# Performance work log

Hardware: AMD Instinct MI355X
Metric: run time of the kernel (lower is better)

Reference implementation:

```python
import jax, jax.numpy as jnp
import numpy as np
import math


def setup_inputs() -> dict:
    key = jax.random.key(0)
    k1, k2, k3, k4 = jax.random.split(key, 4)
    B, L, H, D = 2, 4096, 8, 64
    factor = 5
    U = factor * int(np.ceil(np.log(L)))  # 45 = sample_k = n_top
    return {
        "queries": jax.random.normal(k1, (B, L, H, D), dtype=jnp.float32),
        "keys": jax.random.normal(k2, (B, L, H, D), dtype=jnp.float32),
        "values": jax.random.normal(k3, (B, L, H, D), dtype=jnp.float32),
        "index_sample": jax.random.randint(k4, (L, U), 0, L),  # sampled key ids per query
    }


def reference(queries, keys, values, index_sample):
    # ProbAttention forward, mask_flag=False (non-causal ProbSparse attention).
    B, L_Q, H, D = queries.shape
    L_K = keys.shape[1]
    Q = jnp.transpose(queries, (0, 2, 1, 3))  # (B,H,L_Q,D)
    K = jnp.transpose(keys, (0, 2, 1, 3))     # (B,H,L_K,D)
    V = jnp.transpose(values, (0, 2, 1, 3))   # (B,H,L_K,D)
    n_top = index_sample.shape[1]             # U = factor*ceil(ln(L_K)) = sample_k = n_top

    # --- _prob_QK: score each query against a random subset of keys ---
    K_sample = K[:, :, index_sample, :]                     # (B,H,L_Q,sample_k,D)
    Q_K_sample = jnp.einsum('bhqd,bhqsd->bhqs', Q, K_sample)
    # sparsity measure M = max - mean (sum divided by full L_K, as in source)
    M = Q_K_sample.max(-1) - Q_K_sample.sum(-1) / L_K       # (B,H,L_Q)
    _, M_top = jax.lax.top_k(M, n_top)                      # (B,H,n_top)

    # full attention scores only for the selected top queries
    Q_reduce = jnp.take_along_axis(Q, M_top[..., None], axis=2)  # (B,H,n_top,D)
    scale = 1.0 / math.sqrt(D)
    scores = jnp.einsum('bhud,bhkd->bhuk', Q_reduce, K) * scale  # (B,H,n_top,L_K)
    attn = jax.nn.softmax(scores, axis=-1)

    # --- initial context (mask_flag=False): cumulative sum of V ---
    context = jnp.cumsum(V, axis=2)                         # (B,H,L_Q,D)

    # --- scatter attention outputs into the top-query rows ---
    update = jnp.einsum('bhuk,bhkd->bhud', attn, V)         # (B,H,n_top,D)
    bi = jnp.arange(B)[:, None, None]
    hi = jnp.arange(H)[None, :, None]
    context = context.at[bi, hi, M_top].set(update)

    return jnp.transpose(context, (0, 2, 1, 3))             # (B,L_Q,H,D)
```

## Files before the change

### kernel.cpp

```cpp
#include <hip/hip_runtime.h>
#include <math.h>

#define BB 2
#define LL 4096
#define HH 8
#define DD 64
#define UU 45
#define TILE 128
#define NTILES (LL / TILE)

#define NC 64
#define CK (LL / NC)
#define KSTR 68
#define SSTR 68

__device__ __forceinline__ int qkv_idx(int b, int l, int h, int d) {
    return ((b * LL + l) * HH + h) * DD + d;
}

__global__ __launch_bounds__(256) void k_computeM(
        const float* __restrict__ Q, const float* __restrict__ K,
        const int* __restrict__ idx, float* __restrict__ M) {
    int w = (blockIdx.x * blockDim.x + threadIdx.x) >> 6;
    int lane = threadIdx.x & 63;
    int q = w % LL;
    int bh = w / LL;
    int h = bh % HH, b = bh / HH;

    const float* Kbh = K + (size_t)(b * LL * HH + h) * DD;
    const size_t rowStride = (size_t)HH * DD;

    float qv = Q[qkv_idx(b, q, h, lane)];
    int myks = idx[q * UU + (lane < UU ? lane : 0)];

    int r = lane >> 4;
    int c16 = lane & 15;

    float q0 = __shfl(qv, c16 * 4 + 0, 64);
    float q1 = __shfl(qv, c16 * 4 + 1, 64);
    float q2 = __shfl(qv, c16 * 4 + 2, 64);
    float q3 = __shfl(qv, c16 * 4 + 3, 64);

    float mval = -INFINITY, sval = 0.f;
#pragma unroll
    for (int g = 0; g < 12; ++g) {
        int s = g * 4 + r;
        int ks = __shfl(myks, s, 64);
        const float4* kp = (const float4*)(Kbh + (size_t)ks * rowStride);
        float4 kk = kp[c16];
        float part = fmaf(kk.x, q0, fmaf(kk.y, q1, fmaf(kk.z, q2, kk.w * q3)));
        part += __shfl_xor(part, 8, 64);
        part += __shfl_xor(part, 4, 64);
        part += __shfl_xor(part, 2, 64);
        part += __shfl_xor(part, 1, 64);
        if (s < UU) { mval = fmaxf(mval, part); sval += part; }
    }
    mval = fmaxf(mval, __shfl_xor(mval, 16, 64));
    sval += __shfl_xor(sval, 16, 64);
    mval = fmaxf(mval, __shfl_xor(mval, 32, 64));
    sval += __shfl_xor(sval, 32, 64);
    if (lane == 0) M[bh * LL + q] = mval - sval * (1.0f / LL);
}

__global__ __launch_bounds__(1024) void k_topk(
        const float* __restrict__ M, int* __restrict__ Mtop) {
    int bh = blockIdx.x;
    int t = threadIdx.x;
    __shared__ unsigned keys[LL];
    __shared__ unsigned hist[256];
    __shared__ unsigned scanbuf[256];
    __shared__ unsigned sPrefix, sMask, sK, sBin;
    __shared__ int outCount, eqCount;
    __shared__ int eqIdx[64];

    for (int i = t; i < LL; i += 1024) {
        unsigned u = __float_as_uint(M[bh * LL + i]);
        keys[i] = (u & 0x80000000u) ? ~u : (u | 0x80000000u);
    }
    if (t == 0) { sPrefix = 0u; sMask = 0u; sK = UU; outCount = 0; eqCount = 0; }
    __syncthreads();

    for (int pass = 0; pass < 4; ++pass) {
        int shift = 24 - pass * 8;
        if (t < 256) hist[t] = 0u;
        __syncthreads();
        unsigned prefix = sPrefix, mask = sMask;
        for (int i = t; i < LL; i += 1024) {
            unsigned k = keys[i];
            if ((k & mask) == prefix)
                atomicAdd(&hist[(k >> shift) & 0xFFu], 1u);
        }
        __syncthreads();
        if (t < 256) scanbuf[t] = hist[t];
        __syncthreads();
        for (int off = 1; off < 256; off <<= 1) {
            unsigned v = 0u;
            if (t < 256 && t + off < 256) v = scanbuf[t + off];
            __syncthreads();
            if (t < 256) scanbuf[t] += v;
            __syncthreads();
        }
        if (t < 256) {
            unsigned k = sK;
            unsigned geq = scanbuf[t];
            unsigned gt = (t < 255) ? scanbuf[t + 1] : 0u;
            if (gt < k && geq >= k) sBin = (unsigned)t;
        }
        __syncthreads();
        if (t == 0) {
            unsigned b = sBin;
            unsigned gt = (b < 255u) ? scanbuf[b + 1] : 0u;
            sK -= gt;
            sPrefix |= (b << shift);
            sMask |= (0xFFu << shift);
        }
        __syncthreads();
    }
    unsigned T = sPrefix;
    int kEq = (int)sK;

    for (int i = t; i < LL; i += 1024) {
        unsigned k = keys[i];
        if (k > T) {
            int slot = atomicAdd(&outCount, 1);
            Mtop[bh * UU + slot] = i;
        } else if (k == T) {
            int e = atomicAdd(&eqCount, 1);
            if (e < 64) eqIdx[e] = i;
        }
    }
    __syncthreads();

    if (t == 0) {
        int base = outCount;
        int ec = eqCount;
        if (ec <= 64) {
            for (int s = 0; s < UU; ++s) {
                if (s >= kEq) break;
                int bi = -1, bv = LL + 2;
                for (int j = 0; j < ec; ++j) {
                    int v = eqIdx[j];
                    if (v < bv) { bv = v; bi = j; }
                }
                Mtop[bh * UU + base + s] = bv;
                eqIdx[bi] = LL + 2;
            }
        } else {
            int got = 0;
            for (int i = 0; i < LL && got < kEq; ++i)
                if (keys[i] == T) { Mtop[bh * UU + base + got] = i; ++got; }
        }
    }
}

__global__ __launch_bounds__(256) void k_tilesum(
        const float* __restrict__ V, float* __restrict__ tsum) {
    int blk = blockIdx.x;
    int tile = blk % NTILES;
    int bh = blk / NTILES;
    int h = bh % HH, b = bh / HH;
    int d = threadIdx.x & 63, g = threadIdx.x >> 6;
    const int CH = TILE / 4;
    int l0 = tile * TILE + g * CH;
    float acc = 0.f;
    for (int i = 0; i < CH; ++i) acc += V[qkv_idx(b, l0 + i, h, d)];
    __shared__ float red[4][DD];
    red[g][d] = acc;
    __syncthreads();
    if (g == 0) tsum[blk * DD + d] = red[0][d] + red[1][d] + red[2][d] + red[3][d];
}

__global__ void k_scantiles(float* __restrict__ tsum) {
    int bh = blockIdx.x;
    int d = threadIdx.x;
    float off = 0.f;
    for (int t = 0; t < NTILES; ++t) {
        int i = (bh * NTILES + t) * DD + d;
        float v = tsum[i];
        tsum[i] = off;
        off += v;
    }
}

__global__ __launch_bounds__(256) void k_cumsum(
        const float* __restrict__ V, const float* __restrict__ tsum,
        float* __restrict__ out) {
    int blk = blockIdx.x;
    int tile = blk % NTILES;
    int bh = blk / NTILES;
    int h = bh % HH, b = bh / HH;
    int d = threadIdx.x & 63, g = threadIdx.x >> 6;
    const int CH = TILE / 4;
    int l0 = tile * TILE + g * CH;

    __shared__ float red[4][DD];
    float acc = 0.f;
    for (int i = 0; i < CH; ++i) acc += V[qkv_idx(b, l0 + i, h, d)];
    red[g][d] = acc;
    __syncthreads();

    float off = tsum[blk * DD + d];
    for (int gg = 0; gg < g; ++gg) off += red[gg][d];

    float run = off;
    for (int i = 0; i < CH; ++i) {
        run += V[qkv_idx(b, l0 + i, h, d)];
        out[qkv_idx(b, l0 + i, h, d)] = run;
    }
}

__global__ __launch_bounds__(256) void k_attn_partial(
        const float* __restrict__ Q, const float* __restrict__ K,
        const float* __restrict__ V, const int* __restrict__ Mtop,
        float* __restrict__ mPart, float* __restrict__ lPart,
        float* __restrict__ Op) {
    int blk = blockIdx.x;
    int c = blk % NC;
    int bh = blk / NC;
    int h = bh % HH, b = bh / HH;
    int k0 = c * CK;
    int t = threadIdx.x;

    __shared__ float Qs[48 * KSTR];
    __shared__ float Ks[CK * KSTR];
    __shared__ float Ss[UU * SSTR];

    const size_t rowStride = (size_t)HH * DD;
    const float* Qbh = Q + (size_t)(b * LL * HH + h) * DD;
    const float* Kbh = K + (size_t)(b * LL * HH + h) * DD;
    const float* Vbh = V + (size_t)(b * LL * HH + h) * DD;

    for (int p = t; p < 48 * DD; p += 256) {
        int u = p >> 6, d = p & 63;
        float v = 0.f;
        if (u < UU) {
            int qi = Mtop[bh * UU + u];
            v = Qbh[(size_t)qi * rowStride + d] * 0.125f;
        }
        Qs[u * KSTR + d] = v;
    }
    for (int p = t; p < CK * 16; p += 256) {
        int row = p >> 4, i = p & 15;
        *(float4*)&Ks[row * KSTR + i * 4] =
            *(const float4*)&Kbh[(size_t)(k0 + row) * rowStride + i * 4];
    }
    __syncthreads();

    int kq = t & 15, uq = t >> 4;
    int u0 = uq * 3;
    float acc[3][4];
#pragma unroll
    for (int i = 0; i < 3; ++i)
#pragma unroll
        for (int j = 0; j < 4; ++j) acc[i][j] = 0.f;

#pragma unroll 4
    for (int dd = 0; dd < 16; ++dd) {
        float4 qf[3];
#pragma unroll
        for (int i = 0; i < 3; ++i)
            qf[i] = *(const float4*)&Qs[(u0 + i) * KSTR + dd * 4];
        float4 kf[4];
#pragma unroll
        for (int j = 0; j < 4; ++j)
            kf[j] = *(const float4*)&Ks[(kq + 16 * j) * KSTR + dd * 4];
#pragma unroll
        for (int i = 0; i < 3; ++i)
#pragma unroll
            for (int j = 0; j < 4; ++j) {
                acc[i][j] = fmaf(qf[i].x, kf[j].x, acc[i][j]);
                acc[i][j] = fmaf(qf[i].y, kf[j].y, acc[i][j]);
                acc[i][j] = fmaf(qf[i].z, kf[j].z, acc[i][j]);
                acc[i][j] = fmaf(qf[i].w, kf[j].w, acc[i][j]);
            }
    }
#pragma unroll
    for (int i = 0; i < 3; ++i) {
        int u = u0 + i;
        if (u < UU)
#pragma unroll
            for (int j = 0; j < 4; ++j) Ss[u * SSTR + kq + 16 * j] = acc[i][j];
    }
    __syncthreads();

    for (int p = t; p < CK * 16; p += 256) {
        int row = p >> 4, i = p & 15;
        *(float4*)&Ks[row * KSTR + i * 4] =
            *(const float4*)&Vbh[(size_t)(k0 + row) * rowStride + i * 4];
    }

    if (t < UU * 4) {
        int u = t >> 2, qq = t & 3;
        float mloc = -INFINITY;
        for (int j = 0; j < CK / 4; ++j)
            mloc = fmaxf(mloc, Ss[u * SSTR + qq + 4 * j]);
        mloc = fmaxf(mloc, __shfl_xor(mloc, 1, 64));
        mloc = fmaxf(mloc, __shfl_xor(mloc, 2, 64));
        float lloc = 0.f;
        for (int j = 0; j < CK / 4; ++j) {
            int kk = qq + 4 * j;
            float e = __expf(Ss[u * SSTR + kk] - mloc);
            Ss[u * SSTR + kk] = e;
            lloc += e;
        }
        lloc += __shfl_xor(lloc, 1, 64);
        lloc += __shfl_xor(lloc, 2, 64);
        if (qq == 0) {
            mPart[(bh * NC + c) * UU + u] = mloc;
            lPart[(bh * NC + c) * UU + u] = lloc;
        }
    }
    __syncthreads();

    int dq = t & 15;
    int d0 = dq * 4;
    if (u0 < UU) {
        float4 o[3];
#pragma unroll
        for (int i = 0; i < 3; ++i) o[i] = make_float4(0.f, 0.f, 0.f, 0.f);
#pragma unroll 4
        for (int kc = 0; kc < CK / 4; ++kc) {
            float4 vk[4];
#pragma unroll
            for (int jj = 0; jj < 4; ++jj)
                vk[jj] = *(const float4*)&Ks[(4 * kc + jj) * KSTR + d0];
#pragma unroll
            for (int i = 0; i < 3; ++i) {
                float4 pf = *(const float4*)&Ss[(u0 + i) * SSTR + 4 * kc];
                o[i].x = fmaf(pf.x, vk[0].x, o[i].x);
                o[i].y = fmaf(pf.x, vk[0].y, o[i].y);
                o[i].z = fmaf(pf.x, vk[0].z, o[i].z);
                o[i].w = fmaf(pf.x, vk[0].w, o[i].w);
                o[i].x = fmaf(pf.y, vk[1].x, o[i].x);
                o[i].y = fmaf(pf.y, vk[1].y, o[i].y);
                o[i].z = fmaf(pf.y, vk[1].z, o[i].z);
                o[i].w = fmaf(pf.y, vk[1].w, o[i].w);
                o[i].x = fmaf(pf.z, vk[2].x, o[i].x);
                o[i].y = fmaf(pf.z, vk[2].y, o[i].y);
                o[i].z = fmaf(pf.z, vk[2].z, o[i].z);
                o[i].w = fmaf(pf.z, vk[2].w, o[i].w);
                o[i].x = fmaf(pf.w, vk[3].x, o[i].x);
                o[i].y = fmaf(pf.w, vk[3].y, o[i].y);
                o[i].z = fmaf(pf.w, vk[3].z, o[i].z);
                o[i].w = fmaf(pf.w, vk[3].w, o[i].w);
            }
        }
#pragma unroll
        for (int i = 0; i < 3; ++i) {
            int u = u0 + i;
            *(float4*)&Op[((size_t)(bh * NC + c) * UU + u) * DD + d0] = o[i];
        }
    }
}

__global__ void k_attn_combine(
        const int* __restrict__ Mtop, const float* __restrict__ mPart,
        const float* __restrict__ lPart, const float* __restrict__ Op,
        float* __restrict__ out) {
    int blk = blockIdx.x;
    int u = blk % UU;
    int bh = blk / UU;
    int h = bh % HH, b = bh / HH;
    int d = threadIdx.x;
    float gm = -INFINITY;
    for (int c = 0; c < NC; ++c)
        gm = fmaxf(gm, mPart[(bh * NC + c) * UU + u]);
    float denom = 0.f, acc = 0.f;
    for (int c = 0; c < NC; ++c) {
        int pi = (bh * NC + c) * UU + u;
        float w = __expf(mPart[pi] - gm);
        denom = fmaf(lPart[pi], w, denom);
        acc = fmaf(w, Op[(size_t)pi * DD + d], acc);
    }
    int qi = Mtop[bh * UU + u];
    out[qkv_idx(b, qi, h, d)] = acc / denom;
}

__global__ __launch_bounds__(256) void k_attn_mono(
        const float* __restrict__ Q, const float* __restrict__ K,
        const float* __restrict__ V, const int* __restrict__ Mtop,
        float* __restrict__ out) {
    int blk = blockIdx.x;
    int u = blk % UU;
    int bh = blk / UU;
    int h = bh % HH, b = bh / HH;
    int qi = Mtop[bh * UU + u];
    int t = threadIdx.x;

    __shared__ float scores[LL];
    __shared__ float red[256];

    const float4* qp = (const float4*)(Q + qkv_idx(b, qi, h, 0));
    float4 qreg[16];
#pragma unroll
    for (int i = 0; i < 16; ++i) {
        float4 v = qp[i];
        v.x *= 0.125f; v.y *= 0.125f; v.z *= 0.125f; v.w *= 0.125f;
        qreg[i] = v;
    }

    float lmax = -INFINITY;
    for (int k = t; k < LL; k += 256) {
        const float4* kr = (const float4*)(K + qkv_idx(b, k, h, 0));
        float dot = 0.f;
#pragma unroll
        for (int i = 0; i < 16; ++i) {
            float4 kk = kr[i];
            dot = fmaf(qreg[i].x, kk.x, dot);
            dot = fmaf(qreg[i].y, kk.y, dot);
            dot = fmaf(qreg[i].z, kk.z, dot);
            dot = fmaf(qreg[i].w, kk.w, dot);
        }
        scores[k] = dot;
        lmax = fmaxf(lmax, dot);
    }
    red[t] = lmax;
    __syncthreads();
    for (int off = 128; off >= 1; off >>= 1) {
        if (t < off) red[t] = fmaxf(red[t], red[t + off]);
        __syncthreads();
    }
    float smax = red[0];
    __syncthreads();

    float lsum = 0.f;
    for (int k = t; k < LL; k += 256) {
        float e = __expf(scores[k] - smax);
        scores[k] = e;
        lsum += e;
    }
    red[t] = lsum;
    __syncthreads();
    for (int off = 128; off >= 1; off >>= 1) {
        if (t < off) red[t] += red[t + off];
        __syncthreads();
    }
    float denom = red[0];
    __syncthreads();

    int d = t & 63, g = t >> 6;
    const float4* sc4 = (const float4*)scores;
    float acc = 0.f;
    for (int kb = g; kb < LL / 4; kb += 4) {
        float4 s4 = sc4[kb];
        int kk0 = kb * 4;
        acc = fmaf(s4.x, V[qkv_idx(b, kk0 + 0, h, d)], acc);
        acc = fmaf(s4.y, V[qkv_idx(b, kk0 + 1, h, d)], acc);
        acc = fmaf(s4.z, V[qkv_idx(b, kk0 + 2, h, d)], acc);
        acc = fmaf(s4.w, V[qkv_idx(b, kk0 + 3, h, d)], acc);
    }
    red[t] = acc;
    __syncthreads();
    if (g == 0) {
        float s = red[d] + red[64 + d] + red[128 + d] + red[192 + d];
        out[qkv_idx(b, qi, h, d)] = s / denom;
    }
}

extern "C" void kernel_launch(void* const* d_in, const int* in_sizes, int n_in,
                              void* d_out, int out_size, void* d_ws, size_t ws_size,
                              hipStream_t stream) {
    const float* Q = (const float*)d_in[0];
    const float* K = (const float*)d_in[1];
    const float* V = (const float*)d_in[2];
    const int* idx = (const int*)d_in[3];
    float* out = (float*)d_out;

    float* ws = (float*)d_ws;

    const size_t M_off = 0;
    const size_t tsum_off = 65536;
    const size_t mP_off = 98304;
    const size_t lP_off = 144384;
    const size_t top_off = 190464;
    const size_t Op_off = 191488;
    const size_t need = (Op_off + (size_t)BB * HH * NC * UU * DD) * 4;

    float* M = ws + M_off;
    float* tsum = ws + tsum_off;

    if (ws_size >= need) {
        float* mPart = ws + mP_off;
        float* lPart = ws + lP_off;
        int* Mtop = (int*)(ws + top_off);
        float* Op = ws + Op_off;

        k_computeM<<<BB * HH * LL / 4, 256, 0, stream>>>(Q, K, idx, M);
        k_topk<<<BB * HH, 1024, 0, stream>>>(M, Mtop);
        k_attn_partial<<<BB * HH * NC, 256, 0, stream>>>(Q, K, V, Mtop,
                                                         mPart, lPart, Op);
        k_tilesum<<<BB * HH * NTILES, 256, 0, stream>>>(V, tsum);
        k_scantiles<<<BB * HH, 64, 0, stream>>>(tsum);
        k_cumsum<<<BB * HH * NTILES, 256, 0, stream>>>(V, tsum, out);
        k_attn_combine<<<BB * HH * UU, 64, 0, stream>>>(Mtop, mPart, lPart,
                                                        Op, out);
    } else {
        int* Mtop = (int*)(ws + 65536);
        float* tsum2 = ws + 65536 + 1024;
        k_computeM<<<BB * HH * LL / 4, 256, 0, stream>>>(Q, K, idx, M);
        k_topk<<<BB * HH, 1024, 0, stream>>>(M, Mtop);
        k_tilesum<<<BB * HH * NTILES, 256, 0, stream>>>(V, tsum2);
        k_scantiles<<<BB * HH, 64, 0, stream>>>(tsum2);
        k_cumsum<<<BB * HH * NTILES, 256, 0, stream>>>(V, tsum2, out);
        k_attn_mono<<<BB * HH * UU, 256, 0, stream>>>(Q, K, V, Mtop, out);
    }
}
```

Measured before the change: 209.6 us.

## Drop tile-scan kernel and skip cumsum writes for selected query rows

Removes the serial k_scantiles launch. Each cumsum block now computes its own tile prefix by summing the preceding tile sums in-kernel. The top-k kernel also builds a bitmap of selected query rows, and cumsum runs after combine, skipping stores to rows the attention output already wrote. This saves one launch and a serial pass, in exchange for redundant prefix summation (up to 31 tiles per block) and an extra bitmap read.

```diff
diff --git a/kernel.cpp b/kernel.cpp
--- a/kernel.cpp
+++ b/kernel.cpp
@@ -63,7 +63,8 @@
 }
 
 __global__ __launch_bounds__(1024) void k_topk(
-        const float* __restrict__ M, int* __restrict__ Mtop) {
+        const float* __restrict__ M, int* __restrict__ Mtop,
+        unsigned* __restrict__ selmap) {
     int bh = blockIdx.x;
     int t = threadIdx.x;
     __shared__ unsigned keys[LL];
@@ -77,6 +78,7 @@
         unsigned u = __float_as_uint(M[bh * LL + i]);
         keys[i] = (u & 0x80000000u) ? ~u : (u | 0x80000000u);
     }
+    if (selmap != nullptr && t < 128) selmap[bh * 128 + t] = 0u;
     if (t == 0) { sPrefix = 0u; sMask = 0u; sK = UU; outCount = 0; eqCount = 0; }
     __syncthreads();
 
@@ -151,6 +153,11 @@
                 if (keys[i] == T) { Mtop[bh * UU + base + got] = i; ++got; }
         }
     }
+    __syncthreads();
+    if (selmap != nullptr && t < UU) {
+        int qi = Mtop[bh * UU + t];
+        atomicOr(&selmap[bh * 128 + (qi >> 5)], 1u << (qi & 31));
+    }
 }
 
 __global__ __launch_bounds__(256) void k_tilesum(
@@ -170,42 +177,41 @@
     if (g == 0) tsum[blk * DD + d] = red[0][d] + red[1][d] + red[2][d] + red[3][d];
 }
 
-__global__ void k_scantiles(float* __restrict__ tsum) {
-    int bh = blockIdx.x;
-    int d = threadIdx.x;
-    float off = 0.f;
-    for (int t = 0; t < NTILES; ++t) {
-        int i = (bh * NTILES + t) * DD + d;
-        float v = tsum[i];
-        tsum[i] = off;
-        off += v;
-    }
-}
-
 __global__ __launch_bounds__(256) void k_cumsum(
         const float* __restrict__ V, const float* __restrict__ tsum,
-        float* __restrict__ out) {
+        const unsigned* __restrict__ selmap, float* __restrict__ out) {
     int blk = blockIdx.x;
     int tile = blk % NTILES;
     int bh = blk / NTILES;
     int h = bh % HH, b = bh / HH;
-    int d = threadIdx.x & 63, g = threadIdx.x >> 6;
+    int t = threadIdx.x;
+    int d = t & 63, g = t >> 6;
     const int CH = TILE / 4;
     int l0 = tile * TILE + g * CH;
 
     __shared__ float red[4][DD];
+    __shared__ float pref[DD];
     float acc = 0.f;
     for (int i = 0; i < CH; ++i) acc += V[qkv_idx(b, l0 + i, h, d)];
     red[g][d] = acc;
-    __syncthreads();
-
-    float off = tsum[blk * DD + d];
+    if (t < DD) {
+        float off = 0.f;
+        for (int tt = 0; tt < tile; ++tt)
+            off += tsum[(bh * NTILES + tt) * DD + t];
+        pref[t] = off;
+    }
+    __syncthreads();
+
+    float off = pref[d];
     for (int gg = 0; gg < g; ++gg) off += red[gg][d];
+
+    unsigned selw = (selmap != nullptr) ? selmap[bh * 128 + (l0 >> 5)] : 0u;
 
     float run = off;
     for (int i = 0; i < CH; ++i) {
         run += V[qkv_idx(b, l0 + i, h, d)];
-        out[qkv_idx(b, l0 + i, h, d)] = run;
+        if (!((selw >> i) & 1u))
+            out[qkv_idx(b, l0 + i, h, d)] = run;
     }
 }
 
@@ -473,7 +479,8 @@
     const size_t mP_off = 98304;
     const size_t lP_off = 144384;
     const size_t top_off = 190464;
-    const size_t Op_off = 191488;
+    const size_t sel_off = 191488;
+    const size_t Op_off = 193536;
     const size_t need = (Op_off + (size_t)BB * HH * NC * UU * DD) * 4;
 
     float* M = ws + M_off;
@@ -483,25 +490,26 @@
         float* mPart = ws + mP_off;
         float* lPart = ws + lP_off;
         int* Mtop = (int*)(ws + top_off);
+        unsigned* selmap = (unsigned*)(ws + sel_off);
         float* Op = ws + Op_off;
 
         k_computeM<<<BB * HH * LL / 4, 256, 0, stream>>>(Q, K, idx, M);
-        k_topk<<<BB * HH, 1024, 0, stream>>>(M, Mtop);
+        k_topk<<<BB * HH, 1024, 0, stream>>>(M, Mtop, selmap);
         k_attn_partial<<<BB * HH * NC, 256, 0, stream>>>(Q, K, V, Mtop,
                                                          mPart, lPart, Op);
         k_tilesum<<<BB * HH * NTILES, 256, 0, stream>>>(V, tsum);
-        k_scantiles<<<BB * HH, 64, 0, stream>>>(tsum);
-        k_cumsum<<<BB * HH * NTILES, 256, 0, stream>>>(V, tsum, out);
         k_attn_combine<<<BB * HH * UU, 64, 0, stream>>>(Mtop, mPart, lPart,
                                                         Op, out);
+        k_cumsum<<<BB * HH * NTILES, 256, 0, stream>>>(V, tsum, selmap, out);
     } else {
         int* Mtop = (int*)(ws + 65536);
         float* tsum2 = ws + 65536 + 1024;
         k_computeM<<<BB * HH * LL / 4, 256, 0, stream>>>(Q, K, idx, M);
-        k_topk<<<BB * HH, 1024, 0, stream>>>(M, Mtop);
+        k_topk<<<BB * HH, 1024, 0, stream>>>(M, Mtop, (unsigned*)nullptr);
         k_tilesum<<<BB * HH * NTILES, 256, 0, stream>>>(V, tsum2);
-        k_scantiles<<<BB * HH, 64, 0, stream>>>(tsum2);
-        k_cumsum<<<BB * HH * NTILES, 256, 0, stream>>>(V, tsum2, out);
+        k_cumsum<<<BB * HH * NTILES, 256, 0, stream>>>(V, tsum2,
+                                                       (const unsigned*)nullptr,
+                                                       out);
         k_attn_mono<<<BB * HH * UU, 256, 0, stream>>>(Q, K, V, Mtop, out);
     }
 }
```

Measured after the change: 219.6 us. 4.8% more time.
